# Kernel tuning notes

Hardware: AMD Instinct MI355X
Metric: run time of the kernel (lower is better)

The kernel has to match this reference:

```python
import jax, jax.numpy as jnp
import numpy as np

D = 256        # input_dim / embed_dim
H = 128        # hidden_dim
NH = 8         # attention heads
S = 64         # number of superpoint segments
LN_EPS = 1e-5
CW = 0.3       # consistency weight


def layernorm(x, g, b):
    m = jnp.mean(x, axis=-1, keepdims=True)
    v = jnp.var(x, axis=-1, keepdims=True)
    return (x - m) * jax.lax.rsqrt(v + LN_EPS) * g + b


def mlp(x, w1, b1, g1, be1, w2, b2, g2, be2):
    # Linear -> LayerNorm -> ReLU -> Linear -> LayerNorm (torch Sequential)
    h = jax.nn.relu(layernorm(x @ w1.T + b1, g1, be1))
    return layernorm(h @ w2.T + b2, g2, be2)


def setup_inputs() -> dict:
    key = jax.random.key(0)
    ks = jax.random.split(key, 16)
    B, N = 2, 512
    p = {}
    p['coordinates'] = jax.random.normal(ks[0], (B, N, 3), dtype=jnp.float32)
    p['features'] = jax.random.normal(ks[1], (B, N, D), dtype=jnp.float32)
    p['superpoint_labels'] = jax.random.randint(ks[2], (B, N), 0, S, dtype=jnp.int32)
    sc = 0.02
    # geometric_encoder: Linear(9,H), LN(H), ReLU, Linear(H,D), LN(D)
    p['ge_w1'] = jax.random.normal(ks[3], (H, 9), dtype=jnp.float32) * sc
    p['ge_b1'] = jnp.zeros((H,), jnp.float32)
    p['ge_g1'] = jnp.ones((H,), jnp.float32)
    p['ge_be1'] = jnp.zeros((H,), jnp.float32)
    p['ge_w2'] = jax.random.normal(ks[4], (D, H), dtype=jnp.float32) * sc
    p['ge_b2'] = jnp.zeros((D,), jnp.float32)
    p['ge_g2'] = jnp.ones((D,), jnp.float32)
    p['ge_be2'] = jnp.zeros((D,), jnp.float32)
    # superpoint_aggregator: Linear(D,H), LN(H), ReLU, Linear(H,D), LN(D)
    p['ag_w1'] = jax.random.normal(ks[5], (H, D), dtype=jnp.float32) * sc
    p['ag_b1'] = jnp.zeros((H,), jnp.float32)
    p['ag_g1'] = jnp.ones((H,), jnp.float32)
    p['ag_be1'] = jnp.zeros((H,), jnp.float32)
    p['ag_w2'] = jax.random.normal(ks[6], (D, H), dtype=jnp.float32) * sc
    p['ag_b2'] = jnp.zeros((D,), jnp.float32)
    p['ag_g2'] = jnp.ones((D,), jnp.float32)
    p['ag_be2'] = jnp.zeros((D,), jnp.float32)
    # MultiheadAttention projections (torch [out,in] layout)
    p['wq'] = jax.random.normal(ks[7], (D, D), dtype=jnp.float32) * sc
    p['bq'] = jnp.zeros((D,), jnp.float32)
    p['wk'] = jax.random.normal(ks[8], (D, D), dtype=jnp.float32) * sc
    p['bk'] = jnp.zeros((D,), jnp.float32)
    p['wv'] = jax.random.normal(ks[9], (D, D), dtype=jnp.float32) * sc
    p['bv'] = jnp.zeros((D,), jnp.float32)
    p['wo'] = jax.random.normal(ks[10], (D, D), dtype=jnp.float32) * sc
    p['bo'] = jnp.zeros((D,), jnp.float32)
    return p


def reference(coordinates, features, superpoint_labels,
              ge_w1, ge_b1, ge_g1, ge_be1, ge_w2, ge_b2, ge_g2, ge_be2,
              ag_w1, ag_b1, ag_g1, ag_be1, ag_w2, ag_b2, ag_g2, ag_be2,
              wq, bq, wk, bk, wv, bv, wo, bo):
    B, N, Dm = features.shape
    # pairwise geometric features [B,N,N,*]
    rel = coordinates[:, :, None, :] - coordinates[:, None, :, :]
    dist = jnp.linalg.norm(rel, axis=-1, keepdims=True)
    rn = rel / jnp.maximum(dist, 1e-12)  # F.normalize semantics
    r0, r1, r2 = rn[..., 0], rn[..., 1], rn[..., 2]
    z = jnp.zeros_like(r0)
    # torch code writes to channels -2, -1, 2 of 5 => [0, 0, r1*r2, r0*r1, r0*r2]
    ang = jnp.stack([z, z, r1 * r2, r0 * r1, r0 * r2], axis=-1)
    geo_rel = jnp.concatenate([dist, rn, ang], axis=-1)  # [B,N,N,9]
    enc = mlp(geo_rel, ge_w1, ge_b1, ge_g1, ge_be1, ge_w2, ge_b2, ge_g2, ge_be2)
    geo_ctx = jnp.mean(enc, axis=2)  # [B,N,D]

    # vectorized per-superpoint segment mean + aggregator + scatter-back
    def per_batch(feat, geo, lab):
        ones = jnp.ones(lab.shape, feat.dtype)
        cnt = jax.ops.segment_sum(ones, lab, num_segments=S)          # [S]
        denom = jnp.maximum(cnt, 1.0)[:, None]
        mf = jax.ops.segment_sum(feat, lab, num_segments=S) / denom  # [S,D]
        mg = jax.ops.segment_sum(geo, lab, num_segments=S) / denom   # [S,D]
        agg = mlp(mf, ag_w1, ag_b1, ag_g1, ag_be1, ag_w2, ag_b2, ag_g2, ag_be2)
        comb = agg + mg
        upd = (1.0 - CW) * feat + CW * comb[lab]
        keep = (cnt >= 2.0)[lab][:, None]  # groups with <2 points untouched
        return jnp.where(keep, upd, feat)

    enhanced = jax.vmap(per_batch)(features, geo_ctx, superpoint_labels)

    # MultiheadAttention(q=enhanced, k=v=geo_ctx)
    hd = Dm // NH
    scale = np.float32(1.0 / np.sqrt(hd))
    q = (enhanced @ wq.T + bq).reshape(B, N, NH, hd).transpose(0, 2, 1, 3)
    k = (geo_ctx @ wk.T + bk).reshape(B, N, NH, hd).transpose(0, 2, 1, 3)
    v = (geo_ctx @ wv.T + bv).reshape(B, N, NH, hd).transpose(0, 2, 1, 3)
    attn = jax.nn.softmax(jnp.einsum('bhqd,bhkd->bhqk', q, k) * scale, axis=-1)
    o = jnp.einsum('bhqk,bhkd->bhqd', attn, v).transpose(0, 2, 1, 3).reshape(B, N, Dm)
    spatial = o @ wo.T + bo
    return enhanced + 0.5 * spatial
```

## Files before the change

### kernel.cpp

```cpp
#include <hip/hip_runtime.h>

#define NPTS 512
#define DIM  256
#define HID  128
#define NSEG 64
#define LN_EPS 1e-5f
#define KTS 520

typedef short s16x4 __attribute__((ext_vector_type(4)));
typedef short s16x8 __attribute__((ext_vector_type(8)));
typedef float f32x4 __attribute__((ext_vector_type(4)));
typedef const float* fpc;

__device__ __forceinline__ unsigned short f2bf(float f) {
  unsigned int u = __builtin_bit_cast(unsigned int, f);
  u += 0x7FFFu + ((u >> 16) & 1u);
  return (unsigned short)(u >> 16);
}

__global__ void k02_prep_agg(
    fpc ge_w1, fpc ge_b1, fpc ge_w2, fpc ge_b2,
    fpc features, const int* __restrict__ labels,
    fpc wk, fpc wv, fpc wq, fpc wo,
    fpc ag_w1, fpc ag_b1, fpc ag_g1, fpc ag_be1,
    fpc ag_w2, fpc ag_b2, fpc ag_g2, fpc ag_be2,
    unsigned short* __restrict__ gmw, float* __restrict__ uw,
    float* __restrict__ tvw, float* __restrict__ scw, float* __restrict__ qfw,
    float* __restrict__ wkT, float* __restrict__ wvT,
    float* __restrict__ wqT, float* __restrict__ woT,
    float* __restrict__ comb, float* __restrict__ cntf, float* __restrict__ mgsum)
{
  const int blk = blockIdx.x;
  const int t = threadIdx.x;
  if (blk < 130) {
    if (t < 128) {
      if (blk < 128) {
        const int c = blk;
        float acc = 0.f;
        for (int d = 0; d < DIM; ++d) acc += ge_w2[d * HID + c] * ge_w2[d * HID + t];
        gmw[c * HID + t] = f2bf(acc);
      } else if (blk == 128) {
        float uu = 0.f, tv = 0.f;
        for (int d = 0; d < DIM; ++d) { const float w = ge_w2[d * HID + t]; uu += w; tv += ge_b2[d] * w; }
        uw[t] = uu; tvw[t] = tv;
        if (t == 0) {
          float s = 0.f, s2 = 0.f;
          for (int d = 0; d < DIM; ++d) { const float bb = ge_b2[d]; s += bb; s2 += bb * bb; }
          scw[0] = s; scw[1] = s2;
        }
      } else {
        if (t < 101) {
          float acc = 0.f;
          if (t < 81) {
            const int a = t / 9, c = t % 9;
            for (int h = 0; h < HID; ++h) acc += ge_w1[h * 9 + a] * ge_w1[h * 9 + c];
            qfw[a * 12 + c] = acc;
          } else if (t < 90) {
            const int a = t - 81;
            for (int h = 0; h < HID; ++h) acc += ge_w1[h * 9 + a];
            qfw[108 + a] = acc;
          } else if (t < 99) {
            const int a = t - 90;
            for (int h = 0; h < HID; ++h) acc += ge_b1[h] * ge_w1[h * 9 + a];
            qfw[117 + a] = acc;
          } else if (t == 99) {
            float acc2 = 0.f;
            for (int h = 0; h < HID; ++h) acc2 += ge_b1[h];
            qfw[126] = acc2;
          } else {
            float acc2 = 0.f;
            for (int h = 0; h < HID; ++h) acc2 += ge_b1[h] * ge_b1[h];
            qfw[127] = acc2;
          }
        }
      }
    }
    return;
  }
  if (blk < 162) {
    __shared__ __align__(16) float T[32][256];
    const int tr = blk - 130;
    const int m = tr >> 3;
    fpc src = (m == 0) ? wk : (m == 1) ? wv : (m == 2) ? wq : wo;
    float* dst = (m == 0) ? wkT : (m == 1) ? wvT : (m == 2) ? wqT : woT;
    const int c0 = (tr & 7) * 32;
    for (int i = 0; i < 32; ++i) T[i][t] = src[(c0 + i) * DIM + t];
    __syncthreads();
    #pragma unroll
    for (int j4 = 0; j4 < 32; j4 += 4) {
      f32x4 v;
      v[0] = T[j4 + 0][t]; v[1] = T[j4 + 1][t];
      v[2] = T[j4 + 2][t]; v[3] = T[j4 + 3][t];
      *(f32x4*)&dst[t * DIM + c0 + j4] = v;
    }
    return;
  }
  const int item = blk - 162;
  const int lane = t & 63;
  const int wid = t >> 6;
  const int b = item >> 6;
  const int s = item & 63;
  __shared__ __align__(16) int labS[NPTS];
  __shared__ __align__(16) float mfS[DIM];
  __shared__ __align__(16) float h1S[HID];
  __shared__ __align__(16) float red[8];
  mgsum[(b * NSEG + s) * DIM + t] = 0.f;
  for (int n = t; n < NPTS; n += 256) labS[n] = labels[b * NPTS + n];
  __syncthreads();
  float accf = 0.f;
  int cnt = 0;
  for (int n = 0; n < NPTS; n += 4) {
    const int4 l4 = *(const int4*)&labS[n];
    if (l4.x == s) { cnt++; accf += features[(b * NPTS + n + 0) * DIM + t]; }
    if (l4.y == s) { cnt++; accf += features[(b * NPTS + n + 1) * DIM + t]; }
    if (l4.z == s) { cnt++; accf += features[(b * NPTS + n + 2) * DIM + t]; }
    if (l4.w == s) { cnt++; accf += features[(b * NPTS + n + 3) * DIM + t]; }
  }
  const float denom = fmaxf((float)cnt, 1.f);
  mfS[t] = accf / denom;
  __syncthreads();
  float hval = 0.f;
  if (t < HID) {
    float o = ag_b1[t];
    for (int k = 0; k < DIM; k += 4) {
      const f32x4 x = *(const f32x4*)&mfS[k];
      const f32x4 w = *(const f32x4*)&ag_w1[t * DIM + k];
      o += x[0] * w[0] + x[1] * w[1] + x[2] * w[2] + x[3] * w[3];
    }
    hval = o;
  }
  float sv = (t < HID) ? hval : 0.f;
  float qv = (t < HID) ? hval * hval : 0.f;
  #pragma unroll
  for (int off = 1; off < 64; off <<= 1) { sv += __shfl_xor(sv, off); qv += __shfl_xor(qv, off); }
  if (lane == 0 && wid < 2) { red[wid * 2] = sv; red[wid * 2 + 1] = qv; }
  __syncthreads();
  if (t < HID) {
    const float s1 = red[0] + red[2], q1 = red[1] + red[3];
    const float mean = s1 * (1.f / 128.f);
    const float var = fmaxf(q1 * (1.f / 128.f) - mean * mean, 0.f);
    const float rs = rsqrtf(var + LN_EPS);
    h1S[t] = fmaxf((hval - mean) * rs * ag_g1[t] + ag_be1[t], 0.f);
  }
  __syncthreads();
  float o = ag_b2[t];
  for (int k = 0; k < HID; k += 4) {
    const f32x4 x = *(const f32x4*)&h1S[k];
    const f32x4 w = *(const f32x4*)&ag_w2[t * HID + k];
    o += x[0] * w[0] + x[1] * w[1] + x[2] * w[2] + x[3] * w[3];
  }
  float sv2 = o, qv2 = o * o;
  #pragma unroll
  for (int off = 1; off < 64; off <<= 1) { sv2 += __shfl_xor(sv2, off); qv2 += __shfl_xor(qv2, off); }
  if (lane == 0) { red[wid * 2] = sv2; red[wid * 2 + 1] = qv2; }
  __syncthreads();
  const float sa = red[0] + red[2] + red[4] + red[6];
  const float qa = red[1] + red[3] + red[5] + red[7];
  const float mean = sa * (1.f / 256.f);
  const float var = fmaxf(qa * (1.f / 256.f) - mean * mean, 0.f);
  const float rs = rsqrtf(var + LN_EPS);
  comb[(b * NSEG + s) * DIM + t] = (o - mean) * rs * ag_g2[t] + ag_be2[t];
  if (t == 0) cntf[b * NSEG + s] = (float)cnt;
}

__global__ __launch_bounds__(512, 4) void k1_geo(
    fpc coords, const int* __restrict__ labels,
    fpc g1, fpc be1, fpc w1, fpc b1,
    fpc w2, fpc b2, fpc g2, fpc be2,
    fpc wkT, fpc bk, fpc wvT, fpc bv,
    const unsigned short* __restrict__ gmw, fpc uw, fpc tvw, fpc scw, fpc qfw,
    float* __restrict__ Kt, float* __restrict__ Vout, float* __restrict__ mgsum)
{
  const int t = threadIdx.x;
  const int lane = t & 63;
  const int w = t >> 6;
  const int mtw = w >> 2;
  const int cg = w & 3;
  const int bi = blockIdx.x;
  const int b = bi >> 9;

  __shared__ __align__(16) float xs[NPTS][8];
  __shared__ __align__(16) float st[NPTS][2];
  __shared__ __align__(16) float qf[128];
  __shared__ __align__(16) unsigned short h1s[32][136];
  __shared__ __align__(16) float red2[32][12];
  __shared__ __align__(16) float haS[2][128];
  __shared__ __align__(16) float gS[256];
  __shared__ float srsP[2], srmP[2];

  if (t < 128) qf[t] = qfw[t];

  float w1r[2][7], b1r[2], g1r[2], be1r[2];
  #pragma unroll
  for (int r = 0; r < 2; ++r) {
    const int hh = lane * 2 + r;
    w1r[r][0] = w1[hh * 9 + 0]; w1r[r][1] = w1[hh * 9 + 1];
    w1r[r][2] = w1[hh * 9 + 2]; w1r[r][3] = w1[hh * 9 + 3];
    w1r[r][4] = w1[hh * 9 + 6]; w1r[r][5] = w1[hh * 9 + 7];
    w1r[r][6] = w1[hh * 9 + 8];
    b1r[r] = b1[hh]; g1r[r] = g1[hh]; be1r[r] = be1[hh];
  }
  const int n16 = lane & 15;
  const int q16 = lane >> 4;
  const int colc0 = cg * 32 + n16;
  s16x8 gfrag[2][4];
  float u_c[2], tv_c[2];
  #pragma unroll
  for (int dt = 0; dt < 2; ++dt) {
    const int c = colc0 + dt * 16;
    u_c[dt] = uw[c];
    tv_c[dt] = 2.f * tvw[c];
    #pragma unroll
    for (int kt = 0; kt < 4; ++kt)
      gfrag[dt][kt] = *(const s16x8*)&gmw[c * HID + kt * 32 + q16 * 8];
  }
  const float sb = scw[0], sb2 = scw[1];
  const float cix = coords[bi * 3 + 0];
  const float ciy = coords[bi * 3 + 1];
  const float ciz = coords[bi * 3 + 2];
  __syncthreads();

  {
    const int j = t;
    const float cjx = coords[(b * NPTS + j) * 3 + 0];
    const float cjy = coords[(b * NPTS + j) * 3 + 1];
    const float cjz = coords[(b * NPTS + j) * 3 + 2];
    const float rx = cix - cjx, ry = ciy - cjy, rz = ciz - cjz;
    const float dist = sqrtf(rx * rx + ry * ry + rz * rz);
    const float inv = 1.f / fmaxf(dist, 1e-12f);
    const float r0 = rx * inv, r1 = ry * inv, r2 = rz * inv;
    const float x0 = dist, x1 = r0, x2 = r1, x3 = r2;
    const float x6 = r1 * r2, x7 = r0 * r1, x8 = r0 * r2;
    float S1 = qf[126] + qf[108] * x0 + qf[109] * x1 + qf[110] * x2 + qf[111] * x3
             + qf[114] * x6 + qf[115] * x7 + qf[116] * x8;
    float tx = qf[117] * x0 + qf[118] * x1 + qf[119] * x2 + qf[120] * x3
             + qf[123] * x6 + qf[124] * x7 + qf[125] * x8;
    const float xv[9] = {x0, x1, x2, x3, 0.f, 0.f, x6, x7, x8};
    float quad = 0.f;
    #pragma unroll
    for (int a = 0; a < 9; ++a) {
      if (a == 4 || a == 5) continue;
      const f32x4 q0 = *(const f32x4*)&qf[a * 12];
      const f32x4 q1 = *(const f32x4*)&qf[a * 12 + 4];
      const f32x4 q2 = *(const f32x4*)&qf[a * 12 + 8];
      const float ya = q0[0] * x0 + q0[1] * x1 + q0[2] * x2 + q0[3] * x3
                     + q1[2] * x6 + q1[3] * x7 + q2[0] * x8;
      quad += ya * xv[a];
    }
    const float S2 = quad + 2.f * tx + qf[127];
    const float mean = S1 * (1.f / 128.f);
    const float var = fmaxf(S2 * (1.f / 128.f) - mean * mean, 0.f);
    st[j][0] = mean;
    st[j][1] = rsqrtf(var + LN_EPS);
    f32x4 X0; X0[0] = x0; X0[1] = x1; X0[2] = x2; X0[3] = x3;
    f32x4 X1; X1[0] = x6; X1[1] = x7; X1[2] = x8; X1[3] = 0.f;
    *(f32x4*)&xs[j][0] = X0;
    *(f32x4*)&xs[j][4] = X1;
  }
  __syncthreads();

  float haL[2] = {0.f, 0.f};
  float srs = 0.f, srm = 0.f;
  const bool own = (cg == 0) && (n16 == 0);

  for (int jb = 0; jb < NPTS; jb += 32) {
    #pragma unroll
    for (int sr = 0; sr < 4; ++sr) {
      const int m = sr * 8 + w;
      const int j = jb + m;
      const f32x4 X0 = *(const f32x4*)&xs[j][0];
      const f32x4 X1 = *(const f32x4*)&xs[j][4];
      const float2 ms = *(const float2*)&st[j][0];
      unsigned int pk = 0;
      #pragma unroll
      for (int r = 0; r < 2; ++r) {
        const float a = b1r[r]
          + X0[0] * w1r[r][0] + X0[1] * w1r[r][1] + X0[2] * w1r[r][2] + X0[3] * w1r[r][3]
          + X1[0] * w1r[r][4] + X1[1] * w1r[r][5] + X1[2] * w1r[r][6];
        const float e = (a - ms.x) * ms.y * g1r[r] + be1r[r];
        pk |= ((unsigned int)f2bf(fmaxf(e, 0.f))) << (16 * r);
      }
      *(unsigned int*)&h1s[m][lane * 2] = pk;
    }
    __syncthreads();
    f32x4 acc2[2];
    #pragma unroll
    for (int dt = 0; dt < 2; ++dt) {
      f32x4 z; z[0] = tv_c[dt]; z[1] = tv_c[dt]; z[2] = tv_c[dt]; z[3] = tv_c[dt];
      acc2[dt] = z;
    }
    #pragma unroll
    for (int kt = 0; kt < 4; ++kt) {
      const s16x8 af = *(const s16x8*)&h1s[mtw * 16 + n16][kt * 32 + q16 * 8];
      #pragma unroll
      for (int dt = 0; dt < 2; ++dt)
        acc2[dt] = __builtin_amdgcn_mfma_f32_16x16x32_bf16(af, gfrag[dt][kt], acc2[dt], 0, 0, 0);
    }
    float h1v[2][4];
    #pragma unroll
    for (int dt = 0; dt < 2; ++dt)
      #pragma unroll
      for (int r = 0; r < 4; ++r) {
        const unsigned short hv = h1s[mtw * 16 + q16 * 4 + r][colc0 + dt * 16];
        h1v[dt][r] = __builtin_bit_cast(float, ((unsigned int)hv) << 16);
      }
    float sR[4], qR[4];
    #pragma unroll
    for (int r = 0; r < 4; ++r) {
      sR[r] = u_c[0] * h1v[0][r] + u_c[1] * h1v[1][r];
      qR[r] = acc2[0][r] * h1v[0][r] + acc2[1][r] * h1v[1][r];
    }
    #pragma unroll
    for (int off = 1; off < 16; off <<= 1)
      #pragma unroll
      for (int r = 0; r < 4; ++r) {
        sR[r] += __shfl_xor(sR[r], off);
        qR[r] += __shfl_xor(qR[r], off);
      }
    if (n16 == 0)
      #pragma unroll
      for (int r = 0; r < 4; ++r) {
        red2[mtw * 16 + q16 * 4 + r][cg * 2 + 0] = sR[r];
        red2[mtw * 16 + q16 * 4 + r][cg * 2 + 1] = qR[r];
      }
    __syncthreads();
    #pragma unroll
    for (int r = 0; r < 4; ++r) {
      const int row = mtw * 16 + q16 * 4 + r;
      const f32x4 p0 = *(const f32x4*)&red2[row][0];
      const f32x4 p1 = *(const f32x4*)&red2[row][4];
      const float s = p0[0] + p0[2] + p1[0] + p1[2];
      const float q = p0[1] + p0[3] + p1[1] + p1[3];
      const float mean = (s + sb) * (1.f / 256.f);
      const float var = fmaxf((q + sb2) * (1.f / 256.f) - mean * mean, 0.f);
      const float rs = rsqrtf(var + LN_EPS);
      haL[0] += rs * h1v[0][r];
      haL[1] += rs * h1v[1][r];
      if (own) { srs += rs; srm += rs * mean; }
    }
  }

  haL[0] += __shfl_xor(haL[0], 16); haL[0] += __shfl_xor(haL[0], 32);
  haL[1] += __shfl_xor(haL[1], 16); haL[1] += __shfl_xor(haL[1], 32);
  float sa = srs, sm = srm;
  sa += __shfl_xor(sa, 16); sa += __shfl_xor(sa, 32);
  sm += __shfl_xor(sm, 16); sm += __shfl_xor(sm, 32);
  if (lane == 0 && cg == 0) { srsP[mtw] = sa; srmP[mtw] = sm; }
  if (lane < 16) { haS[mtw][colc0] = haL[0]; haS[mtw][colc0 + 16] = haL[1]; }
  __syncthreads();
  if (t < 128) haS[0][t] += haS[1][t];
  __syncthreads();
  const float srsT = srsP[0] + srsP[1];
  const float srmT = srmP[0] + srmP[1];
  if (t < 256) {
    float dot = 0.f;
    for (int k = 0; k < HID; k += 4) {
      const f32x4 wv4 = *(const f32x4*)&w2[t * HID + k];
      const f32x4 h = *(const f32x4*)&haS[0][k];
      dot += wv4[0] * h[0] + wv4[1] * h[1] + wv4[2] * h[2] + wv4[3] * h[3];
    }
    const float gv = (dot + b2[t] * srsT - srmT) * (1.f / 512.f) * g2[t] + be2[t];
    gS[t] = gv;
    atomicAdd(&mgsum[(b * NSEG + labels[bi]) * DIM + t], gv);
  }
  __syncthreads();
  if (t < 256) {
    float kacc = bk[t];
    for (int k = 0; k < DIM; k += 4) {
      const f32x4 g4 = *(const f32x4*)&gS[k];
      kacc += g4[0] * wkT[(k + 0) * DIM + t] + g4[1] * wkT[(k + 1) * DIM + t]
            + g4[2] * wkT[(k + 2) * DIM + t] + g4[3] * wkT[(k + 3) * DIM + t];
    }
    Kt[((b * 8 + (t >> 5)) * 32 + (t & 31)) * KTS + (bi & 511)] = kacc;
  } else {
    const int c = t - 256;
    float vacc = bv[c];
    for (int k = 0; k < DIM; k += 4) {
      const f32x4 g4 = *(const f32x4*)&gS[k];
      vacc += g4[0] * wvT[(k + 0) * DIM + c] + g4[1] * wvT[(k + 1) * DIM + c]
            + g4[2] * wvT[(k + 2) * DIM + c] + g4[3] * wvT[(k + 3) * DIM + c];
    }
    Vout[bi * DIM + c] = vacc;
  }
}

__global__ __launch_bounds__(256, 4) void k5_fused(
    fpc features, const int* __restrict__ labels,
    fpc comb, fpc cntf, fpc mgsum,
    fpc Kt, fpc V, fpc wqT, fpc bq, fpc woT, fpc bo,
    float* __restrict__ out)
{
  const int row = blockIdx.x;
  const int b = row >> 9;
  const int t = threadIdx.x;
  const int w = t >> 6;
  const int l = t & 63;
  __shared__ __align__(16) float E[256];
  __shared__ __align__(16) float Qs[256];
  __shared__ __align__(16) float Px[4][512];
  __shared__ __align__(16) float OcS[256];

  {
    const int lab = labels[row];
    const float cn = cntf[b * NSEG + lab];
    const float f = features[row * DIM + t];
    float v = f;
    if (cn >= 2.f) {
      const float ag = comb[(b * NSEG + lab) * DIM + t];
      const float mg = mgsum[(b * NSEG + lab) * DIM + t];
      v = 0.7f * f + 0.3f * (ag + mg / cn);
    }
    E[t] = v;
  }
  __syncthreads();
  {
    const int c4 = w * 64 + (l & 15) * 4;
    const int k0 = (l >> 4) * 64;
    f32x4 q4 = {0.f, 0.f, 0.f, 0.f};
    for (int k = k0; k < k0 + 64; ++k) {
      const float e = E[k];
      const f32x4 wv4 = *(const f32x4*)&wqT[k * DIM + c4];
      #pragma unroll
      for (int i = 0; i < 4; ++i) q4[i] += e * wv4[i];
    }
    #pragma unroll
    for (int i = 0; i < 4; ++i) { q4[i] += __shfl_xor(q4[i], 16); q4[i] += __shfl_xor(q4[i], 32); }
    if (l < 16) {
      const f32x4 bq4 = *(const f32x4*)&bq[c4];
      f32x4 o;
      #pragma unroll
      for (int i = 0; i < 4; ++i) o[i] = q4[i] + bq4[i];
      *(f32x4*)&Qs[c4] = o;
    }
  }
  for (int hi = 0; hi < 2; ++hi) {
    const int h = w * 2 + hi;
    f32x4 s4[2] = {{0.f, 0.f, 0.f, 0.f}, {0.f, 0.f, 0.f, 0.f}};
    const long kbase = (long)((b * 8 + h) * 32) * KTS;
    for (int d = 0; d < 32; ++d) {
      const float qd = Qs[h * 32 + d];
      const fpc kr = &Kt[kbase + (long)d * KTS];
      const f32x4 k0v = *(const f32x4*)&kr[l * 4];
      const f32x4 k1v = *(const f32x4*)&kr[256 + l * 4];
      #pragma unroll
      for (int i = 0; i < 4; ++i) { s4[0][i] += qd * k0v[i]; s4[1][i] += qd * k1v[i]; }
    }
    #pragma unroll
    for (int i = 0; i < 4; ++i) {
      s4[0][i] *= 0.1767766952966369f;
      s4[1][i] *= 0.1767766952966369f;
    }
    float mx = s4[0][0];
    #pragma unroll
    for (int i = 1; i < 4; ++i) mx = fmaxf(mx, s4[0][i]);
    #pragma unroll
    for (int i = 0; i < 4; ++i) mx = fmaxf(mx, s4[1][i]);
    #pragma unroll
    for (int off = 1; off < 64; off <<= 1) mx = fmaxf(mx, __shfl_xor(mx, off));
    f32x4 p0, p1;
    float sum = 0.f;
    #pragma unroll
    for (int i = 0; i < 4; ++i) { p0[i] = __expf(s4[0][i] - mx); sum += p0[i]; }
    #pragma unroll
    for (int i = 0; i < 4; ++i) { p1[i] = __expf(s4[1][i] - mx); sum += p1[i]; }
    #pragma unroll
    for (int off = 1; off < 64; off <<= 1) sum += __shfl_xor(sum, off);
    const float ri = 1.f / sum;
    #pragma unroll
    for (int i = 0; i < 4; ++i) { p0[i] *= ri; p1[i] *= ri; }
    *(f32x4*)&Px[w][l * 4] = p0;
    *(f32x4*)&Px[w][256 + l * 4] = p1;
    const int j2 = (l & 15) * 2;
    const int k0 = (l >> 4) * 128;
    float o0 = 0.f, o1 = 0.f;
    for (int k = k0; k < k0 + 128; ++k) {
      const float pv = Px[w][k];
      const float2 vv = *(const float2*)&V[(b * NPTS + k) * DIM + h * 32 + j2];
      o0 += pv * vv.x; o1 += pv * vv.y;
    }
    o0 += __shfl_xor(o0, 16); o1 += __shfl_xor(o1, 16);
    o0 += __shfl_xor(o0, 32); o1 += __shfl_xor(o1, 32);
    if (l < 16) { OcS[h * 32 + j2] = o0; OcS[h * 32 + j2 + 1] = o1; }
  }
  __syncthreads();
  {
    const int c4 = w * 64 + (l & 15) * 4;
    const int j0 = (l >> 4) * 64;
    f32x4 d4 = {0.f, 0.f, 0.f, 0.f};
    for (int j = j0; j < j0 + 64; ++j) {
      const float oc = OcS[j];
      const f32x4 wv4 = *(const f32x4*)&woT[j * DIM + c4];
      #pragma unroll
      for (int i = 0; i < 4; ++i) d4[i] += oc * wv4[i];
    }
    #pragma unroll
    for (int i = 0; i < 4; ++i) { d4[i] += __shfl_xor(d4[i], 16); d4[i] += __shfl_xor(d4[i], 32); }
    if (l < 16) {
      const f32x4 bo4 = *(const f32x4*)&bo[c4];
      const f32x4 e4 = *(const f32x4*)&E[c4];
      f32x4 o;
      #pragma unroll
      for (int i = 0; i < 4; ++i) o[i] = e4[i] + 0.5f * (d4[i] + bo4[i]);
      *(f32x4*)&out[row * DIM + c4] = o;
    }
  }
}

extern "C" void kernel_launch(void* const* d_in, const int* in_sizes, int n_in,
                              void* d_out, int out_size, void* d_ws, size_t ws_size,
                              hipStream_t stream)
{
  fpc coords  = (fpc)d_in[0];
  fpc features= (fpc)d_in[1];
  const int* labels = (const int*)d_in[2];
  fpc ge_w1 = (fpc)d_in[3],  ge_b1 = (fpc)d_in[4],  ge_g1 = (fpc)d_in[5],  ge_be1 = (fpc)d_in[6];
  fpc ge_w2 = (fpc)d_in[7],  ge_b2 = (fpc)d_in[8],  ge_g2 = (fpc)d_in[9],  ge_be2 = (fpc)d_in[10];
  fpc ag_w1 = (fpc)d_in[11], ag_b1 = (fpc)d_in[12], ag_g1 = (fpc)d_in[13], ag_be1 = (fpc)d_in[14];
  fpc ag_w2 = (fpc)d_in[15], ag_b2 = (fpc)d_in[16], ag_g2 = (fpc)d_in[17], ag_be2 = (fpc)d_in[18];
  fpc wq = (fpc)d_in[19], bq = (fpc)d_in[20];
  fpc wk = (fpc)d_in[21], bk = (fpc)d_in[22];
  fpc wv = (fpc)d_in[23], bv = (fpc)d_in[24];
  fpc wo = (fpc)d_in[25], bo = (fpc)d_in[26];

  float* ws = (float*)d_ws;
  float* comb    = ws;
  float* cntf    = comb + 32768;
  float* Vb      = cntf + 128;
  float* Ktb     = Vb + 262144;
  float* mgsum   = Ktb + 266240;
  float* gmwF    = mgsum + 32768;
  float* uw      = gmwF + 8192;
  float* tvw     = uw + 128;
  float* scw     = tvw + 128;
  float* qfw     = scw + 8;
  float* wkT     = qfw + 128;
  float* wvT     = wkT + 65536;
  float* wqT     = wvT + 65536;
  float* woT     = wqT + 65536;

  k02_prep_agg<<<290, 256, 0, stream>>>(ge_w1, ge_b1, ge_w2, ge_b2,
                                        features, labels, wk, wv, wq, wo,
                                        ag_w1, ag_b1, ag_g1, ag_be1,
                                        ag_w2, ag_b2, ag_g2, ag_be2,
                                        (unsigned short*)gmwF, uw, tvw, scw, qfw,
                                        wkT, wvT, wqT, woT, comb, cntf, mgsum);
  k1_geo<<<1024, 512, 0, stream>>>(coords, labels, ge_g1, ge_be1, ge_w1, ge_b1,
                                   ge_w2, ge_b2, ge_g2, ge_be2,
                                   wkT, bk, wvT, bv,
                                   (const unsigned short*)gmwF, uw, tvw, scw, qfw,
                                   Ktb, Vb, mgsum);
  k5_fused<<<1024, 256, 0, stream>>>(features, labels, comb, cntf, mgsum,
                                     Ktb, Vb, wqT, bq, woT, bo, (float*)d_out);
}
```

Before: 323.1 us.

## Widen attention kernel to one wave per head and repack geo h1 writes

```diff
diff --git a/kernel.cpp b/kernel.cpp
--- a/kernel.cpp
+++ b/kernel.cpp
@@ -190,10 +190,11 @@
 
   if (t < 128) qf[t] = qfw[t];
 
-  float w1r[2][7], b1r[2], g1r[2], be1r[2];
+  const int ch0 = (t & 31) * 4;
+  float w1r[4][7], b1r[4], g1r[4], be1r[4];
   #pragma unroll
-  for (int r = 0; r < 2; ++r) {
-    const int hh = lane * 2 + r;
+  for (int r = 0; r < 4; ++r) {
+    const int hh = ch0 + r;
     w1r[r][0] = w1[hh * 9 + 0]; w1r[r][1] = w1[hh * 9 + 1];
     w1r[r][2] = w1[hh * 9 + 2]; w1r[r][3] = w1[hh * 9 + 3];
     w1r[r][4] = w1[hh * 9 + 6]; w1r[r][5] = w1[hh * 9 + 7];
@@ -265,22 +266,22 @@
 
   for (int jb = 0; jb < NPTS; jb += 32) {
     #pragma unroll
-    for (int sr = 0; sr < 4; ++sr) {
-      const int m = sr * 8 + w;
+    for (int p = 0; p < 2; ++p) {
+      const int m = p * 16 + (t >> 5);
       const int j = jb + m;
       const f32x4 X0 = *(const f32x4*)&xs[j][0];
       const f32x4 X1 = *(const f32x4*)&xs[j][4];
       const float2 ms = *(const float2*)&st[j][0];
-      unsigned int pk = 0;
-      #pragma unroll
-      for (int r = 0; r < 2; ++r) {
+      s16x4 hn;
+      #pragma unroll
+      for (int r = 0; r < 4; ++r) {
         const float a = b1r[r]
           + X0[0] * w1r[r][0] + X0[1] * w1r[r][1] + X0[2] * w1r[r][2] + X0[3] * w1r[r][3]
           + X1[0] * w1r[r][4] + X1[1] * w1r[r][5] + X1[2] * w1r[r][6];
         const float e = (a - ms.x) * ms.y * g1r[r] + be1r[r];
-        pk |= ((unsigned int)f2bf(fmaxf(e, 0.f))) << (16 * r);
+        hn[r] = (short)f2bf(fmaxf(e, 0.f));
       }
-      *(unsigned int*)&h1s[m][lane * 2] = pk;
+      *(s16x4*)&h1s[m][ch0] = hn;
     }
     __syncthreads();
     f32x4 acc2[2];
@@ -384,7 +385,7 @@
   }
 }
 
-__global__ __launch_bounds__(256, 4) void k5_fused(
+__global__ __launch_bounds__(512, 4) void k5_fused(
     fpc features, const int* __restrict__ labels,
     fpc comb, fpc cntf, fpc mgsum,
     fpc Kt, fpc V, fpc wqT, fpc bq, fpc woT, fpc bo,
@@ -393,14 +394,15 @@
   const int row = blockIdx.x;
   const int b = row >> 9;
   const int t = threadIdx.x;
-  const int w = t >> 6;
+  const int h = t >> 6;
   const int l = t & 63;
   __shared__ __align__(16) float E[256];
   __shared__ __align__(16) float Qs[256];
-  __shared__ __align__(16) float Px[4][512];
+  __shared__ __align__(16) float Px[8][512];
   __shared__ __align__(16) float OcS[256];
-
-  {
+  __shared__ __align__(16) float Wp[512];
+
+  if (t < 256) {
     const int lab = labels[row];
     const float cn = cntf[b * NSEG + lab];
     const float f = features[row * DIM + t];
@@ -414,18 +416,22 @@
   }
   __syncthreads();
   {
-    const int c4 = w * 64 + (l & 15) * 4;
-    const int k0 = (l >> 4) * 64;
+    const int c4 = h * 32 + (l & 7) * 4;
+    const int k0 = (l >> 3) * 32;
     f32x4 q4 = {0.f, 0.f, 0.f, 0.f};
-    for (int k = k0; k < k0 + 64; ++k) {
+    for (int k = k0; k < k0 + 32; ++k) {
       const float e = E[k];
       const f32x4 wv4 = *(const f32x4*)&wqT[k * DIM + c4];
       #pragma unroll
       for (int i = 0; i < 4; ++i) q4[i] += e * wv4[i];
     }
     #pragma unroll
-    for (int i = 0; i < 4; ++i) { q4[i] += __shfl_xor(q4[i], 16); q4[i] += __shfl_xor(q4[i], 32); }
-    if (l < 16) {
+    for (int i = 0; i < 4; ++i) {
+      q4[i] += __shfl_xor(q4[i], 8);
+      q4[i] += __shfl_xor(q4[i], 16);
+      q4[i] += __shfl_xor(q4[i], 32);
+    }
+    if (l < 8) {
       const f32x4 bq4 = *(const f32x4*)&bq[c4];
       f32x4 o;
       #pragma unroll
@@ -433,8 +439,7 @@
       *(f32x4*)&Qs[c4] = o;
     }
   }
-  for (int hi = 0; hi < 2; ++hi) {
-    const int h = w * 2 + hi;
+  {
     f32x4 s4[2] = {{0.f, 0.f, 0.f, 0.f}, {0.f, 0.f, 0.f, 0.f}};
     const long kbase = (long)((b * 8 + h) * 32) * KTS;
     for (int d = 0; d < 32; ++d) {
@@ -468,13 +473,13 @@
     const float ri = 1.f / sum;
     #pragma unroll
     for (int i = 0; i < 4; ++i) { p0[i] *= ri; p1[i] *= ri; }
-    *(f32x4*)&Px[w][l * 4] = p0;
-    *(f32x4*)&Px[w][256 + l * 4] = p1;
+    *(f32x4*)&Px[h][l * 4] = p0;
+    *(f32x4*)&Px[h][256 + l * 4] = p1;
     const int j2 = (l & 15) * 2;
     const int k0 = (l >> 4) * 128;
     float o0 = 0.f, o1 = 0.f;
     for (int k = k0; k < k0 + 128; ++k) {
-      const float pv = Px[w][k];
+      const float pv = Px[h][k];
       const float2 vv = *(const float2*)&V[(b * NPTS + k) * DIM + h * 32 + j2];
       o0 += pv * vv.x; o1 += pv * vv.y;
     }
@@ -484,25 +489,16 @@
   }
   __syncthreads();
   {
-    const int c4 = w * 64 + (l & 15) * 4;
-    const int j0 = (l >> 4) * 64;
-    f32x4 d4 = {0.f, 0.f, 0.f, 0.f};
-    for (int j = j0; j < j0 + 64; ++j) {
-      const float oc = OcS[j];
-      const f32x4 wv4 = *(const f32x4*)&woT[j * DIM + c4];
-      #pragma unroll
-      for (int i = 0; i < 4; ++i) d4[i] += oc * wv4[i];
-    }
-    #pragma unroll
-    for (int i = 0; i < 4; ++i) { d4[i] += __shfl_xor(d4[i], 16); d4[i] += __shfl_xor(d4[i], 32); }
-    if (l < 16) {
-      const f32x4 bo4 = *(const f32x4*)&bo[c4];
-      const f32x4 e4 = *(const f32x4*)&E[c4];
-      f32x4 o;
-      #pragma unroll
-      for (int i = 0; i < 4; ++i) o[i] = e4[i] + 0.5f * (d4[i] + bo4[i]);
-      *(f32x4*)&out[row * DIM + c4] = o;
-    }
+    const int c = t & 255;
+    const int j0 = (t >> 8) * 128;
+    float d = 0.f;
+    for (int j = j0; j < j0 + 128; ++j) d += OcS[j] * woT[j * DIM + c];
+    Wp[t] = d;
+  }
+  __syncthreads();
+  if (t < 256) {
+    const float dd = Wp[t] + Wp[t + 256];
+    out[row * DIM + t] = E[t] + 0.5f * (dd + bo[t]);
   }
 }
 
@@ -549,6 +545,6 @@
                                    wkT, bk, wvT, bv,
                                    (const unsigned short*)gmwF, uw, tvw, scw, qfw,
                                    Ktb, Vb, mgsum);
-  k5_fused<<<1024, 256, 0, stream>>>(features, labels, comb, cntf, mgsum,
+  k5_fused<<<1024, 512, 0, stream>>>(features, labels, comb, cntf, mgsum,
                                      Ktb, Vb, wqT, bq, woT, bo, (float*)d_out);
 }
```

New measurement: 352.2 us. +9.0%, slower.

## Fold prep kernel into geo kernel via atomic work queue, recompute aggregation per row

Applied to the files above, without the earlier changes.

```diff
diff --git a/kernel.cpp b/kernel.cpp
--- a/kernel.cpp
+++ b/kernel.cpp
@@ -7,6 +7,18 @@
 #define LN_EPS 1e-5f
 #define KTS 520
 
+#define IT_GMW0   0
+#define IT_WKT0   32
+#define IT_WVT0   48
+#define IT_UTS    64
+#define IT_QF     65
+#define N_CRIT    66
+#define IT_WQT0   66
+#define IT_WOT0   82
+#define IT_A1T0   98
+#define IT_A2T0   106
+#define NITEMS    122
+
 typedef short s16x4 __attribute__((ext_vector_type(4)));
 typedef short s16x8 __attribute__((ext_vector_type(8)));
 typedef float f32x4 __attribute__((ext_vector_type(4)));
@@ -18,158 +30,19 @@
   return (unsigned short)(u >> 16);
 }
 
-__global__ void k02_prep_agg(
-    fpc ge_w1, fpc ge_b1, fpc ge_w2, fpc ge_b2,
-    fpc features, const int* __restrict__ labels,
-    fpc wk, fpc wv, fpc wq, fpc wo,
-    fpc ag_w1, fpc ag_b1, fpc ag_g1, fpc ag_be1,
-    fpc ag_w2, fpc ag_b2, fpc ag_g2, fpc ag_be2,
+__global__ __launch_bounds__(512, 4) void k1_geo(
+    fpc coords,
+    fpc g1, fpc be1, fpc w1, fpc b1,
+    fpc w2, fpc b2, fpc g2, fpc be2,
+    fpc wk, fpc bk, fpc wv, fpc bv, fpc wq, fpc wo,
+    fpc ag_w1, fpc ag_w2,
     unsigned short* __restrict__ gmw, float* __restrict__ uw,
     float* __restrict__ tvw, float* __restrict__ scw, float* __restrict__ qfw,
     float* __restrict__ wkT, float* __restrict__ wvT,
     float* __restrict__ wqT, float* __restrict__ woT,
-    float* __restrict__ comb, float* __restrict__ cntf, float* __restrict__ mgsum)
-{
-  const int blk = blockIdx.x;
-  const int t = threadIdx.x;
-  if (blk < 130) {
-    if (t < 128) {
-      if (blk < 128) {
-        const int c = blk;
-        float acc = 0.f;
-        for (int d = 0; d < DIM; ++d) acc += ge_w2[d * HID + c] * ge_w2[d * HID + t];
-        gmw[c * HID + t] = f2bf(acc);
-      } else if (blk == 128) {
-        float uu = 0.f, tv = 0.f;
-        for (int d = 0; d < DIM; ++d) { const float w = ge_w2[d * HID + t]; uu += w; tv += ge_b2[d] * w; }
-        uw[t] = uu; tvw[t] = tv;
-        if (t == 0) {
-          float s = 0.f, s2 = 0.f;
-          for (int d = 0; d < DIM; ++d) { const float bb = ge_b2[d]; s += bb; s2 += bb * bb; }
-          scw[0] = s; scw[1] = s2;
-        }
-      } else {
-        if (t < 101) {
-          float acc = 0.f;
-          if (t < 81) {
-            const int a = t / 9, c = t % 9;
-            for (int h = 0; h < HID; ++h) acc += ge_w1[h * 9 + a] * ge_w1[h * 9 + c];
-            qfw[a * 12 + c] = acc;
-          } else if (t < 90) {
-            const int a = t - 81;
-            for (int h = 0; h < HID; ++h) acc += ge_w1[h * 9 + a];
-            qfw[108 + a] = acc;
-          } else if (t < 99) {
-            const int a = t - 90;
-            for (int h = 0; h < HID; ++h) acc += ge_b1[h] * ge_w1[h * 9 + a];
-            qfw[117 + a] = acc;
-          } else if (t == 99) {
-            float acc2 = 0.f;
-            for (int h = 0; h < HID; ++h) acc2 += ge_b1[h];
-            qfw[126] = acc2;
-          } else {
-            float acc2 = 0.f;
-            for (int h = 0; h < HID; ++h) acc2 += ge_b1[h] * ge_b1[h];
-            qfw[127] = acc2;
-          }
-        }
-      }
-    }
-    return;
-  }
-  if (blk < 162) {
-    __shared__ __align__(16) float T[32][256];
-    const int tr = blk - 130;
-    const int m = tr >> 3;
-    fpc src = (m == 0) ? wk : (m == 1) ? wv : (m == 2) ? wq : wo;
-    float* dst = (m == 0) ? wkT : (m == 1) ? wvT : (m == 2) ? wqT : woT;
-    const int c0 = (tr & 7) * 32;
-    for (int i = 0; i < 32; ++i) T[i][t] = src[(c0 + i) * DIM + t];
-    __syncthreads();
-    #pragma unroll
-    for (int j4 = 0; j4 < 32; j4 += 4) {
-      f32x4 v;
-      v[0] = T[j4 + 0][t]; v[1] = T[j4 + 1][t];
-      v[2] = T[j4 + 2][t]; v[3] = T[j4 + 3][t];
-      *(f32x4*)&dst[t * DIM + c0 + j4] = v;
-    }
-    return;
-  }
-  const int item = blk - 162;
-  const int lane = t & 63;
-  const int wid = t >> 6;
-  const int b = item >> 6;
-  const int s = item & 63;
-  __shared__ __align__(16) int labS[NPTS];
-  __shared__ __align__(16) float mfS[DIM];
-  __shared__ __align__(16) float h1S[HID];
-  __shared__ __align__(16) float red[8];
-  mgsum[(b * NSEG + s) * DIM + t] = 0.f;
-  for (int n = t; n < NPTS; n += 256) labS[n] = labels[b * NPTS + n];
-  __syncthreads();
-  float accf = 0.f;
-  int cnt = 0;
-  for (int n = 0; n < NPTS; n += 4) {
-    const int4 l4 = *(const int4*)&labS[n];
-    if (l4.x == s) { cnt++; accf += features[(b * NPTS + n + 0) * DIM + t]; }
-    if (l4.y == s) { cnt++; accf += features[(b * NPTS + n + 1) * DIM + t]; }
-    if (l4.z == s) { cnt++; accf += features[(b * NPTS + n + 2) * DIM + t]; }
-    if (l4.w == s) { cnt++; accf += features[(b * NPTS + n + 3) * DIM + t]; }
-  }
-  const float denom = fmaxf((float)cnt, 1.f);
-  mfS[t] = accf / denom;
-  __syncthreads();
-  float hval = 0.f;
-  if (t < HID) {
-    float o = ag_b1[t];
-    for (int k = 0; k < DIM; k += 4) {
-      const f32x4 x = *(const f32x4*)&mfS[k];
-      const f32x4 w = *(const f32x4*)&ag_w1[t * DIM + k];
-      o += x[0] * w[0] + x[1] * w[1] + x[2] * w[2] + x[3] * w[3];
-    }
-    hval = o;
-  }
-  float sv = (t < HID) ? hval : 0.f;
-  float qv = (t < HID) ? hval * hval : 0.f;
-  #pragma unroll
-  for (int off = 1; off < 64; off <<= 1) { sv += __shfl_xor(sv, off); qv += __shfl_xor(qv, off); }
-  if (lane == 0 && wid < 2) { red[wid * 2] = sv; red[wid * 2 + 1] = qv; }
-  __syncthreads();
-  if (t < HID) {
-    const float s1 = red[0] + red[2], q1 = red[1] + red[3];
-    const float mean = s1 * (1.f / 128.f);
-    const float var = fmaxf(q1 * (1.f / 128.f) - mean * mean, 0.f);
-    const float rs = rsqrtf(var + LN_EPS);
-    h1S[t] = fmaxf((hval - mean) * rs * ag_g1[t] + ag_be1[t], 0.f);
-  }
-  __syncthreads();
-  float o = ag_b2[t];
-  for (int k = 0; k < HID; k += 4) {
-    const f32x4 x = *(const f32x4*)&h1S[k];
-    const f32x4 w = *(const f32x4*)&ag_w2[t * HID + k];
-    o += x[0] * w[0] + x[1] * w[1] + x[2] * w[2] + x[3] * w[3];
-  }
-  float sv2 = o, qv2 = o * o;
-  #pragma unroll
-  for (int off = 1; off < 64; off <<= 1) { sv2 += __shfl_xor(sv2, off); qv2 += __shfl_xor(qv2, off); }
-  if (lane == 0) { red[wid * 2] = sv2; red[wid * 2 + 1] = qv2; }
-  __syncthreads();
-  const float sa = red[0] + red[2] + red[4] + red[6];
-  const float qa = red[1] + red[3] + red[5] + red[7];
-  const float mean = sa * (1.f / 256.f);
-  const float var = fmaxf(qa * (1.f / 256.f) - mean * mean, 0.f);
-  const float rs = rsqrtf(var + LN_EPS);
-  comb[(b * NSEG + s) * DIM + t] = (o - mean) * rs * ag_g2[t] + ag_be2[t];
-  if (t == 0) cntf[b * NSEG + s] = (float)cnt;
-}
-
-__global__ __launch_bounds__(512, 4) void k1_geo(
-    fpc coords, const int* __restrict__ labels,
-    fpc g1, fpc be1, fpc w1, fpc b1,
-    fpc w2, fpc b2, fpc g2, fpc be2,
-    fpc wkT, fpc bk, fpc wvT, fpc bv,
-    const unsigned short* __restrict__ gmw, fpc uw, fpc tvw, fpc scw, fpc qfw,
-    float* __restrict__ Kt, float* __restrict__ Vout, float* __restrict__ mgsum)
+    float* __restrict__ agw1T, float* __restrict__ agw2T,
+    int* __restrict__ ctr,
+    float* __restrict__ geo_ctx, float* __restrict__ Kt, float* __restrict__ Vout)
 {
   const int t = threadIdx.x;
   const int lane = t & 63;
@@ -187,6 +60,130 @@
   __shared__ __align__(16) float haS[2][128];
   __shared__ __align__(16) float gS[256];
   __shared__ float srsP[2], srmP[2];
+  __shared__ int itemS;
+
+  float* TS = &xs[0][0];
+
+  for (;;) {
+    if (t == 0) itemS = __hip_atomic_fetch_add(&ctr[0], 1, __ATOMIC_RELAXED, __HIP_MEMORY_SCOPE_AGENT);
+    __syncthreads();
+    const int item = itemS;
+    __syncthreads();
+    if (item >= NITEMS) break;
+    if (item < IT_WKT0) {
+      const int e = (item << 9) | t;
+      const int c = e >> 7, r = e & 127;
+      float acc = 0.f;
+      for (int d = 0; d < DIM; ++d) acc += w2[d * HID + c] * w2[d * HID + r];
+      gmw[c * HID + r] = f2bf(acc);
+    } else if (item < IT_UTS) {
+      const int s = (item < IT_WVT0) ? item - IT_WKT0 : item - IT_WVT0;
+      fpc src = (item < IT_WVT0) ? wk : wv;
+      float* dst = (item < IT_WVT0) ? wkT : wvT;
+      const int c0 = s * 16;
+      if (t < 256) for (int i = 0; i < 16; ++i) TS[i * 256 + t] = src[(c0 + i) * DIM + t];
+      __syncthreads();
+      if (t < 256) {
+        #pragma unroll
+        for (int j = 0; j < 16; j += 4) {
+          f32x4 v;
+          v[0] = TS[(j + 0) * 256 + t]; v[1] = TS[(j + 1) * 256 + t];
+          v[2] = TS[(j + 2) * 256 + t]; v[3] = TS[(j + 3) * 256 + t];
+          *(f32x4*)&dst[t * DIM + c0 + j] = v;
+        }
+      }
+      __syncthreads();
+    } else if (item == IT_UTS) {
+      if (t < 128) {
+        float uu = 0.f, tv = 0.f;
+        for (int d = 0; d < DIM; ++d) { const float ww = w2[d * HID + t]; uu += ww; tv += b2[d] * ww; }
+        uw[t] = uu; tvw[t] = tv;
+        if (t == 0) {
+          float s = 0.f, s2 = 0.f;
+          for (int d = 0; d < DIM; ++d) { const float bb = b2[d]; s += bb; s2 += bb * bb; }
+          scw[0] = s; scw[1] = s2;
+        }
+      }
+    } else if (item == IT_QF) {
+      if (t < 101) {
+        float acc = 0.f;
+        if (t < 81) {
+          const int a = t / 9, c = t % 9;
+          for (int h = 0; h < HID; ++h) acc += w1[h * 9 + a] * w1[h * 9 + c];
+          qfw[a * 12 + c] = acc;
+        } else if (t < 90) {
+          const int a = t - 81;
+          for (int h = 0; h < HID; ++h) acc += w1[h * 9 + a];
+          qfw[108 + a] = acc;
+        } else if (t < 99) {
+          const int a = t - 90;
+          for (int h = 0; h < HID; ++h) acc += b1[h] * w1[h * 9 + a];
+          qfw[117 + a] = acc;
+        } else if (t == 99) {
+          for (int h = 0; h < HID; ++h) acc += b1[h];
+          qfw[126] = acc;
+        } else {
+          for (int h = 0; h < HID; ++h) acc += b1[h] * b1[h];
+          qfw[127] = acc;
+        }
+      }
+    } else if (item < IT_A1T0) {
+      const int s = (item < IT_WOT0) ? item - IT_WQT0 : item - IT_WOT0;
+      fpc src = (item < IT_WOT0) ? wq : wo;
+      float* dst = (item < IT_WOT0) ? wqT : woT;
+      const int c0 = s * 16;
+      if (t < 256) for (int i = 0; i < 16; ++i) TS[i * 256 + t] = src[(c0 + i) * DIM + t];
+      __syncthreads();
+      if (t < 256) {
+        #pragma unroll
+        for (int j = 0; j < 16; j += 4) {
+          f32x4 v;
+          v[0] = TS[(j + 0) * 256 + t]; v[1] = TS[(j + 1) * 256 + t];
+          v[2] = TS[(j + 2) * 256 + t]; v[3] = TS[(j + 3) * 256 + t];
+          *(f32x4*)&dst[t * DIM + c0 + j] = v;
+        }
+      }
+      __syncthreads();
+    } else if (item < IT_A2T0) {
+      const int c0 = (item - IT_A1T0) * 16;
+      if (t < 256) for (int i = 0; i < 16; ++i) TS[i * 256 + t] = ag_w1[(c0 + i) * DIM + t];
+      __syncthreads();
+      if (t < 256) {
+        #pragma unroll
+        for (int j = 0; j < 16; j += 4) {
+          f32x4 v;
+          v[0] = TS[(j + 0) * 256 + t]; v[1] = TS[(j + 1) * 256 + t];
+          v[2] = TS[(j + 2) * 256 + t]; v[3] = TS[(j + 3) * 256 + t];
+          *(f32x4*)&agw1T[t * HID + c0 + j] = v;
+        }
+      }
+      __syncthreads();
+    } else {
+      const int c0 = (item - IT_A2T0) * 16;
+      if (t < 128) for (int i = 0; i < 16; ++i) TS[i * 128 + t] = ag_w2[(c0 + i) * HID + t];
+      __syncthreads();
+      if (t < 128) {
+        #pragma unroll
+        for (int j = 0; j < 16; j += 4) {
+          f32x4 v;
+          v[0] = TS[(j + 0) * 128 + t]; v[1] = TS[(j + 1) * 128 + t];
+          v[2] = TS[(j + 2) * 128 + t]; v[3] = TS[(j + 3) * 128 + t];
+          *(f32x4*)&agw2T[t * DIM + c0 + j] = v;
+        }
+      }
+      __syncthreads();
+    }
+    __syncthreads();
+    __threadfence();
+    if (t == 0 && item < N_CRIT)
+      __hip_atomic_fetch_add(&ctr[1], 1, __ATOMIC_RELEASE, __HIP_MEMORY_SCOPE_AGENT);
+  }
+  if (t == 0) {
+    while (__hip_atomic_load(&ctr[1], __ATOMIC_ACQUIRE, __HIP_MEMORY_SCOPE_AGENT) < N_CRIT)
+      __builtin_amdgcn_s_sleep(8);
+  }
+  __syncthreads();
+  __threadfence();
 
   if (t < 128) qf[t] = qfw[t];
 
@@ -361,7 +358,7 @@
     }
     const float gv = (dot + b2[t] * srsT - srmT) * (1.f / 512.f) * g2[t] + be2[t];
     gS[t] = gv;
-    atomicAdd(&mgsum[(b * NSEG + labels[bi]) * DIM + t], gv);
+    geo_ctx[bi * DIM + t] = gv;
   }
   __syncthreads();
   if (t < 256) {
@@ -385,9 +382,10 @@
 }
 
 __global__ __launch_bounds__(256, 4) void k5_fused(
-    fpc features, const int* __restrict__ labels,
-    fpc comb, fpc cntf, fpc mgsum,
+    fpc features, const int* __restrict__ labels, fpc geo,
     fpc Kt, fpc V, fpc wqT, fpc bq, fpc woT, fpc bo,
+    fpc agw1T, fpc ag_b1, fpc ag_g1, fpc ag_be1,
+    fpc agw2T, fpc ag_b2, fpc ag_g2, fpc ag_be2,
     float* __restrict__ out)
 {
   const int row = blockIdx.x;
@@ -395,22 +393,79 @@
   const int t = threadIdx.x;
   const int w = t >> 6;
   const int l = t & 63;
+  const int lane = t & 63;
+  const int wid = t >> 6;
+  __shared__ __align__(16) int labS[NPTS];
   __shared__ __align__(16) float E[256];
   __shared__ __align__(16) float Qs[256];
   __shared__ __align__(16) float Px[4][512];
   __shared__ __align__(16) float OcS[256];
-
+  __shared__ __align__(16) float mfS[256];
+  __shared__ __align__(16) float h1S[128];
+  __shared__ __align__(16) float red[8];
+
+  labS[t] = labels[b * NPTS + t];
+  labS[t + 256] = labels[b * NPTS + t + 256];
+  const int lab = labels[row];
+  __syncthreads();
+  float fsum = 0.f, gsum = 0.f;
+  int cnt = 0;
+  const int base = b * NPTS;
+  for (int n = 0; n < NPTS; n += 4) {
+    const int4 l4 = *(const int4*)&labS[n];
+    if (l4.x == lab) { cnt++; fsum += features[(base + n + 0) * DIM + t]; gsum += geo[(base + n + 0) * DIM + t]; }
+    if (l4.y == lab) { cnt++; fsum += features[(base + n + 1) * DIM + t]; gsum += geo[(base + n + 1) * DIM + t]; }
+    if (l4.z == lab) { cnt++; fsum += features[(base + n + 2) * DIM + t]; gsum += geo[(base + n + 2) * DIM + t]; }
+    if (l4.w == lab) { cnt++; fsum += features[(base + n + 3) * DIM + t]; gsum += geo[(base + n + 3) * DIM + t]; }
+  }
+  const float denom = fmaxf((float)cnt, 1.f);
+  mfS[t] = fsum / denom;
+  const float mgd = gsum / denom;
+  __syncthreads();
+  float hval = 0.f;
+  if (t < HID) {
+    float o = ag_b1[t];
+    for (int k = 0; k < DIM; k += 4) {
+      const f32x4 x = *(const f32x4*)&mfS[k];
+      o += x[0] * agw1T[(k + 0) * HID + t] + x[1] * agw1T[(k + 1) * HID + t]
+         + x[2] * agw1T[(k + 2) * HID + t] + x[3] * agw1T[(k + 3) * HID + t];
+    }
+    hval = o;
+  }
+  float sv = (t < HID) ? hval : 0.f;
+  float qv = (t < HID) ? hval * hval : 0.f;
+  #pragma unroll
+  for (int off = 1; off < 64; off <<= 1) { sv += __shfl_xor(sv, off); qv += __shfl_xor(qv, off); }
+  if (lane == 0 && wid < 2) { red[wid * 2] = sv; red[wid * 2 + 1] = qv; }
+  __syncthreads();
+  if (t < HID) {
+    const float s1 = red[0] + red[2], q1 = red[1] + red[3];
+    const float mean = s1 * (1.f / 128.f);
+    const float var = fmaxf(q1 * (1.f / 128.f) - mean * mean, 0.f);
+    const float rs = rsqrtf(var + LN_EPS);
+    h1S[t] = fmaxf((hval - mean) * rs * ag_g1[t] + ag_be1[t], 0.f);
+  }
+  __syncthreads();
+  float o2 = ag_b2[t];
+  for (int k = 0; k < HID; k += 4) {
+    const f32x4 x = *(const f32x4*)&h1S[k];
+    o2 += x[0] * agw2T[(k + 0) * DIM + t] + x[1] * agw2T[(k + 1) * DIM + t]
+        + x[2] * agw2T[(k + 2) * DIM + t] + x[3] * agw2T[(k + 3) * DIM + t];
+  }
+  float sv2 = o2, qv2 = o2 * o2;
+  #pragma unroll
+  for (int off = 1; off < 64; off <<= 1) { sv2 += __shfl_xor(sv2, off); qv2 += __shfl_xor(qv2, off); }
+  if (lane == 0) { red[wid * 2] = sv2; red[wid * 2 + 1] = qv2; }
+  __syncthreads();
   {
-    const int lab = labels[row];
-    const float cn = cntf[b * NSEG + lab];
-    const float f = features[row * DIM + t];
-    float v = f;
-    if (cn >= 2.f) {
-      const float ag = comb[(b * NSEG + lab) * DIM + t];
-      const float mg = mgsum[(b * NSEG + lab) * DIM + t];
-      v = 0.7f * f + 0.3f * (ag + mg / cn);
-    }
-    E[t] = v;
+    const float sa = red[0] + red[2] + red[4] + red[6];
+    const float qa = red[1] + red[3] + red[5] + red[7];
+    const float mean = sa * (1.f / 256.f);
+    const float var = fmaxf(qa * (1.f / 256.f) - mean * mean, 0.f);
+    const float rs = rsqrtf(var + LN_EPS);
+    const float combv = (o2 - mean) * rs * ag_g2[t] + ag_be2[t];
+    const float fv = features[row * DIM + t];
+    E[t] = (cnt >= 2) ? 0.7f * fv + 0.3f * (combv + mgd) : fv;
   }
   __syncthreads();
   {
@@ -523,12 +578,10 @@
   fpc wo = (fpc)d_in[25], bo = (fpc)d_in[26];
 
   float* ws = (float*)d_ws;
-  float* comb    = ws;
-  float* cntf    = comb + 32768;
-  float* Vb      = cntf + 128;
+  float* geo_ctx = ws;
+  float* Vb      = geo_ctx + 262144;
   float* Ktb     = Vb + 262144;
-  float* mgsum   = Ktb + 266240;
-  float* gmwF    = mgsum + 32768;
+  float* gmwF    = Ktb + 266240;
   float* uw      = gmwF + 8192;
   float* tvw     = uw + 128;
   float* scw     = tvw + 128;
@@ -537,18 +590,19 @@
   float* wvT     = wkT + 65536;
   float* wqT     = wvT + 65536;
   float* woT     = wqT + 65536;
-
-  k02_prep_agg<<<290, 256, 0, stream>>>(ge_w1, ge_b1, ge_w2, ge_b2,
-                                        features, labels, wk, wv, wq, wo,
-                                        ag_w1, ag_b1, ag_g1, ag_be1,
-                                        ag_w2, ag_b2, ag_g2, ag_be2,
-                                        (unsigned short*)gmwF, uw, tvw, scw, qfw,
-                                        wkT, wvT, wqT, woT, comb, cntf, mgsum);
-  k1_geo<<<1024, 512, 0, stream>>>(coords, labels, ge_g1, ge_be1, ge_w1, ge_b1,
+  float* agw1T   = woT + 65536;
+  float* agw2T   = agw1T + 32768;
+  int*   ctr     = (int*)(agw2T + 32768);
+
+  hipMemsetAsync(ctr, 0, 2 * sizeof(int), stream);
+  k1_geo<<<1024, 512, 0, stream>>>(coords, ge_g1, ge_be1, ge_w1, ge_b1,
                                    ge_w2, ge_b2, ge_g2, ge_be2,
-                                   wkT, bk, wvT, bv,
-                                   (const unsigned short*)gmwF, uw, tvw, scw, qfw,
-                                   Ktb, Vb, mgsum);
-  k5_fused<<<1024, 256, 0, stream>>>(features, labels, comb, cntf, mgsum,
-                                     Ktb, Vb, wqT, bq, woT, bo, (float*)d_out);
+                                   wk, bk, wv, bv, wq, wo, ag_w1, ag_w2,
+                                   (unsigned short*)gmwF, uw, tvw, scw, qfw,
+                                   wkT, wvT, wqT, woT, agw1T, agw2T, ctr,
+                                   geo_ctx, Ktb, Vb);
+  k5_fused<<<1024, 256, 0, stream>>>(features, labels, geo_ctx,
+                                     Ktb, Vb, wqT, bq, woT, bo,
+                                     agw1T, ag_b1, ag_g1, ag_be1,
+                                     agw2T, ag_b2, ag_g2, ag_be2, (float*)d_out);
 }
```

Result: slower. 572.3 us (+77.2%).
